# Kernel optimization log

Hardware: AMD Instinct MI355X
Metric: run time of the kernel (lower is better)

Reference implementation:

```python
import jax, jax.numpy as jnp
import numpy as np

UNITS = 2048
INPUT_DIM = 2048
BATCH = 8192


def setup_inputs() -> dict:
    key = jax.random.key(0)
    k_x, k_w = jax.random.split(key)
    inputs = jax.random.normal(k_x, (BATCH, INPUT_DIM), dtype=jnp.float32)
    # random_normal initializer in keras defaults to stddev=0.05
    w = jax.random.normal(k_w, (INPUT_DIM, UNITS), dtype=jnp.float32) * 0.05
    b = jnp.zeros((UNITS,), dtype=jnp.float32)
    return {"inputs": inputs, "w": w, "b": b}


def reference(inputs, w, b):
    # matmul + bias
    result = jnp.matmul(inputs, w) + b  # [B, units]
    # per-row: if first element > 0.5, add 1 to whole row, else subtract 1
    cond = result[:, :1] > 0.5  # [B, 1], broadcasts over row
    return jnp.where(cond, result + 1.0, result - 1.0)
```

## Files before the change

kernel.cpp:

```cpp
#include <hip/hip_runtime.h>
#include <hip/hip_bf16.h>
#include <stdint.h>

#define M_DIM 8192
#define N_DIM 2048
#define K_DIM 2048

typedef __attribute__((ext_vector_type(8))) short bf16x8;
typedef __attribute__((ext_vector_type(8))) short short8;
typedef __attribute__((ext_vector_type(4))) float f32x4;

static __device__ __forceinline__ unsigned short f2bf(float f) {
  union { float f; unsigned u; } a; a.f = f;
  unsigned u = a.u;
  u += 0x7FFFu + ((u >> 16) & 1u);
  return (unsigned short)(u >> 16);
}

static __device__ __forceinline__ void async16(void* lds, const void* g) {
  __builtin_amdgcn_global_load_lds(
      (const __attribute__((address_space(1))) unsigned int*)g,
      (__attribute__((address_space(3))) unsigned int*)lds, 16, 0, 0);
}

#define BAR()                                \
  do {                                       \
    asm volatile("" ::: "memory");           \
    __builtin_amdgcn_s_barrier();            \
    asm volatile("" ::: "memory");           \
  } while (0)
#define VMCNT(n) asm volatile("s_waitcnt vmcnt(" #n ")" ::: "memory")

__global__ __launch_bounds__(256) void k_prep(const float* __restrict__ W,
    const float* __restrict__ X, const float* __restrict__ b,
    unsigned short* __restrict__ Wt, unsigned short* __restrict__ Xb,
    float* __restrict__ adj) {
  __shared__ float smem[64 * 65];
  const int t = threadIdx.x;
  if (blockIdx.x < 1024) {
    float (*tile)[65] = (float (*)[65])smem;
    const int bx = blockIdx.x & 31;
    const int by = blockIdx.x >> 5;
    const int n0 = bx * 64, k0 = by * 64;
    #pragma unroll
    for (int i = 0; i < 16; ++i) {
      int lin = i * 256 + t;
      int rr = lin >> 6, c = lin & 63;
      tile[rr][c] = W[(size_t)(k0 + rr) * N_DIM + n0 + c];
    }
    __syncthreads();
    #pragma unroll
    for (int i = 0; i < 16; ++i) {
      int lin = i * 256 + t;
      int rr = lin >> 6, c = lin & 63;
      Wt[(size_t)(n0 + rr) * K_DIM + k0 + c] = f2bf(tile[c][rr]);
    }
  } else {
    float* wlds = smem;
    double* red2 = (double*)(smem + 2048);
    const int m0r = (blockIdx.x - 1024) * 16;
    const int w = t >> 6;
    #pragma unroll
    for (int i = 0; i < 8; ++i)
      wlds[t * 8 + i] = W[(size_t)(t * 8 + i) * N_DIM];
    __syncthreads();
    const float4 wv0 = *(const float4*)&wlds[t * 8];
    const float4 wv1 = *(const float4*)&wlds[t * 8 + 4];
    for (int rr = 0; rr < 16; ++rr) {
      const int m = m0r + rr;
      const float4* xr = (const float4*)(X + (size_t)m * K_DIM);
      float4 x0 = xr[2 * t], x1 = xr[2 * t + 1];
      short8 o;
      o[0] = (short)f2bf(x0.x); o[1] = (short)f2bf(x0.y);
      o[2] = (short)f2bf(x0.z); o[3] = (short)f2bf(x0.w);
      o[4] = (short)f2bf(x1.x); o[5] = (short)f2bf(x1.y);
      o[6] = (short)f2bf(x1.z); o[7] = (short)f2bf(x1.w);
      *(short8*)(Xb + (size_t)m * K_DIM + t * 8) = o;
      double s = (double)x0.x * wv0.x + (double)x0.y * wv0.y +
                 (double)x0.z * wv0.z + (double)x0.w * wv0.w +
                 (double)x1.x * wv1.x + (double)x1.y * wv1.y +
                 (double)x1.z * wv1.z + (double)x1.w * wv1.w;
      #pragma unroll
      for (int off = 32; off > 0; off >>= 1) s += __shfl_down(s, off, 64);
      if ((t & 63) == 0) red2[rr * 4 + w] = s;
    }
    __syncthreads();
    if (t < 16) {
      double tot = red2[t * 4] + red2[t * 4 + 1] + red2[t * 4 + 2] +
                   red2[t * 4 + 3] + (double)b[0];
      adj[m0r + t] = (tot > 0.5) ? 1.0f : -1.0f;
    }
  }
}

__device__ __forceinline__ void stage_unit(char* ldsc,
    const unsigned short* __restrict__ src, int row0, int kt,
    int isB, int sel, int wid, int l) {
  char* base = ldsc + (size_t)(kt & 1) * 65536 + (size_t)isB * 32768;
  #pragma unroll
  for (int j = 0; j < 2; ++j) {
    int s = wid * 2 + j;
    int sub_c = s & 1;
    int idx = s >> 1;
    int sub_r = isB ? ((idx & 1) + (idx >> 1) * 4 + sel * 2)
                    : ((idx & 3) + ((idx & 4) ? 8 : 0) + sel * 4);
    int grow = row0 + sub_r * 16 + (l >> 2);
    int gcol = kt * 64 + sub_c * 32 + (((l & 3) * 8) ^ ((l & 32) >> 1));
    async16(base + (size_t)(sub_r * 2 + sub_c) * 1024,
            src + (size_t)grow * K_DIM + gcol);
  }
}

__global__ __launch_bounds__(512, 1) void k_gemm8(
    const unsigned short* __restrict__ A,
    const unsigned short* __restrict__ B,
    const float* __restrict__ bias,
    const float* __restrict__ adj,
    float* __restrict__ out) {
  __shared__ unsigned short lds[2 * 2 * 256 * 64];
  char* ldsc = (char*)lds;

  const int t = threadIdx.x;
  const int wid = t >> 6, l = t & 63;
  const int wm = wid >> 2, wn = wid & 3;

  const int bid = blockIdx.x;
  const int swz = (bid & 7) * 32 + (bid >> 3);
  const int bm = swz >> 3, bn = swz & 7;
  const int m0 = bm * 256, n0 = bn * 256;

  const int r = l & 15, q = l >> 4;
  const int rdoff = (r * 64 + q * 16) ^ ((r & 8) << 2);

  const char* ab0 = ldsc;
  const char* bb0 = ldsc + 32768;
  const char* ab1 = ldsc + 65536;
  const char* bb1 = ldsc + 98304;

  f32x4 acc[8][4] = {};
  bf16x8 af0[2][4], af1[2][4], bv0[2][2], bv1[2][2];

#define STG(isB, sel, kt) \
  stage_unit(ldsc, (isB) ? B : A, (isB) ? n0 : m0, kt, isB, sel, wid, l)

#define RD_A(DST, MH, AB)                                                   \
  _Pragma("unroll") for (int mi4 = 0; mi4 < 4; ++mi4) {                     \
    const int sub_r = wm * 8 + (MH) * 4 + mi4;                              \
    _Pragma("unroll") for (int ks = 0; ks < 2; ++ks)                        \
      DST[ks][mi4] =                                                        \
          *(const bf16x8*)((AB) + (size_t)(sub_r * 2 + ks) * 1024 + rdoff); \
  }

#define RD_B(DST, NH, BB)                                                   \
  _Pragma("unroll") for (int ni2 = 0; ni2 < 2; ++ni2) {                     \
    const int sub_r = wn * 4 + (NH) * 2 + ni2;                              \
    _Pragma("unroll") for (int ks = 0; ks < 2; ++ks)                        \
      DST[ks][ni2] =                                                        \
          *(const bf16x8*)((BB) + (size_t)(sub_r * 2 + ks) * 1024 + rdoff); \
  }

#define CL(MH, NH, AF, BV)                                                  \
  __builtin_amdgcn_s_setprio(1);                                            \
  _Pragma("unroll") for (int ks = 0; ks < 2; ++ks)                          \
    _Pragma("unroll") for (int mi4 = 0; mi4 < 4; ++mi4)                     \
      _Pragma("unroll") for (int ni2 = 0; ni2 < 2; ++ni2)                   \
        acc[(MH) * 4 + mi4][(NH) * 2 + ni2] =                               \
            __builtin_amdgcn_mfma_f32_16x16x32_bf16(                        \
                AF[ks][mi4], BV[ks][ni2],                                   \
                acc[(MH) * 4 + mi4][(NH) * 2 + ni2], 0, 0, 0);              \
  __builtin_amdgcn_s_setprio(0);

#define STQ(MH, NH)                                                         \
  _Pragma("unroll") for (int mi4 = 0; mi4 < 4; ++mi4)                       \
    _Pragma("unroll") for (int ni2 = 0; ni2 < 2; ++ni2) {                   \
      const int mi = (MH) * 4 + mi4, ni = (NH) * 2 + ni2;                   \
      const int col = n0 + wn * 64 + ni * 16 + r;                           \
      const int rowb = m0 + wm * 128 + mi * 16 + q * 4;                     \
      _Pragma("unroll") for (int j = 0; j < 4; ++j)                         \
        out[(size_t)(rowb + j) * N_DIM + col] =                             \
            acc[mi][ni][j] + bias_r[ni] + adj_r[mi][j];                     \
    }

#define PH(RD_STMT, STG_STMT, CL_STMT, WAIT_STMT)                           \
  {                                                                         \
    RD_STMT;                                                                \
    STG_STMT;                                                               \
    BAR();                                                                  \
    CL_STMT;                                                                \
    WAIT_STMT;                                                              \
    BAR();                                                                  \
  }

  STG(0, 0, 0); STG(1, 0, 0); STG(1, 1, 0); STG(0, 1, 0);
  STG(0, 0, 1); STG(1, 0, 1);
  VMCNT(4);
  BAR();

  for (int i = 0; i < 15; ++i) {
    const int t1 = 2 * i + 1, t2 = 2 * i + 2, t3 = 2 * i + 3;
    PH(RD_A(af0, 0, ab0); RD_B(bv0, 0, bb0), STG(1, 1, t1),
       CL(0, 0, af0, bv0), );
    PH(RD_B(bv1, 1, bb0), STG(0, 1, t1), CL(0, 1, af0, bv1), );
    PH(RD_A(af1, 1, ab0), STG(0, 0, t2), CL(1, 0, af1, bv0), );
    PH(, STG(1, 0, t2), CL(1, 1, af1, bv1), VMCNT(4));
    PH(RD_A(af0, 0, ab1); RD_B(bv0, 0, bb1), STG(1, 1, t2),
       CL(0, 0, af0, bv0), );
    PH(RD_B(bv1, 1, bb1), STG(0, 1, t2), CL(0, 1, af0, bv1), );
    PH(RD_A(af1, 1, ab1), STG(0, 0, t3), CL(1, 0, af1, bv0), );
    PH(, STG(1, 0, t3), CL(1, 1, af1, bv1), VMCNT(4));
  }
  PH(RD_A(af0, 0, ab0); RD_B(bv0, 0, bb0), STG(1, 1, 31),
     CL(0, 0, af0, bv0), );
  PH(RD_B(bv1, 1, bb0), STG(0, 1, 31), CL(0, 1, af0, bv1), );
  PH(RD_A(af1, 1, ab0), , CL(1, 0, af1, bv0), );
  PH(, , CL(1, 1, af1, bv1), VMCNT(0));

  float4 adj_r[8];
  float bias_r[4];
  #pragma unroll
  for (int mi = 0; mi < 8; ++mi)
    adj_r[mi] = *(const float4*)&adj[m0 + wm * 128 + mi * 16 + q * 4];
  #pragma unroll
  for (int ni = 0; ni < 4; ++ni)
    bias_r[ni] = bias[n0 + wn * 64 + ni * 16 + r];

  PH(RD_A(af0, 0, ab1); RD_B(bv0, 0, bb1), , CL(0, 0, af0, bv0); STQ(0, 0), );
  PH(RD_B(bv1, 1, bb1), , CL(0, 1, af0, bv1); STQ(0, 1), );
  PH(RD_A(af1, 1, ab1), , CL(1, 0, af1, bv0); STQ(1, 0), );
  {
    CL(1, 1, af1, bv1);
    STQ(1, 1);
  }

#undef PH
#undef STQ
#undef CL
#undef RD_A
#undef RD_B
#undef STG
}

__global__ __launch_bounds__(256) void k_gemm_f32(const float* __restrict__ X,
    const float* __restrict__ W, const float* __restrict__ b,
    float* __restrict__ out) {
  __shared__ float As[16][16];
  __shared__ float Bs[16][17];
  const int bn = blockIdx.x & 127, bm = blockIdx.x >> 7;
  const int tx = threadIdx.x & 15, ty = threadIdx.x >> 4;
  const int row = bm * 16 + ty, col = bn * 16 + tx;
  float acc = 0.f;
  for (int k0 = 0; k0 < K_DIM; k0 += 16) {
    As[ty][tx] = X[(size_t)row * K_DIM + k0 + tx];
    Bs[ty][tx] = W[(size_t)(k0 + ty) * N_DIM + col];
    __syncthreads();
    #pragma unroll
    for (int kk = 0; kk < 16; ++kk) acc += As[ty][kk] * Bs[kk][tx];
    __syncthreads();
  }
  out[(size_t)row * N_DIM + col] = acc + b[col];
}

__global__ __launch_bounds__(256) void k_rowadj(float* __restrict__ out) {
  const int m = blockIdx.x;
  const float c0 = out[(size_t)m * N_DIM];
  __syncthreads();
  const float a = (c0 > 0.5f) ? 1.0f : -1.0f;
  for (int n = threadIdx.x; n < N_DIM; n += 256)
    out[(size_t)m * N_DIM + n] += a;
}

extern "C" void kernel_launch(void* const* d_in, const int* in_sizes, int n_in,
                              void* d_out, int out_size, void* d_ws, size_t ws_size,
                              hipStream_t stream) {
  const float* X = (const float*)d_in[0];
  const float* W = (const float*)d_in[1];
  const float* b = (const float*)d_in[2];
  float* out = (float*)d_out;

  const size_t XB_OFF   = 0;
  const size_t WT_OFF   = (size_t)M_DIM * K_DIM * 2;
  const size_t ADJ_OFF  = WT_OFF + (size_t)N_DIM * K_DIM * 2;
  const size_t NEED     = ADJ_OFF + (size_t)M_DIM * 4;

  if (ws_size >= NEED) {
    unsigned short* Xb  = (unsigned short*)((char*)d_ws + XB_OFF);
    unsigned short* Wt  = (unsigned short*)((char*)d_ws + WT_OFF);
    float* adj  = (float*)((char*)d_ws + ADJ_OFF);
    k_prep<<<dim3(1536), dim3(256), 0, stream>>>(W, X, b, Wt, Xb, adj);
    k_gemm8<<<dim3((M_DIM / 256) * (N_DIM / 256)), dim3(512), 0, stream>>>(
        Xb, Wt, b, adj, out);
  } else {
    k_gemm_f32<<<dim3((M_DIM / 16) * (N_DIM / 16)), dim3(256), 0, stream>>>(
        X, W, b, out);
    k_rowadj<<<dim3(M_DIM), dim3(256), 0, stream>>>(out);
  }
}
```

Before: 88.54 us.

## Replace 256x256 eight-phase GEMM with 256x128 tile, K=32 steps, higher occupancy

Swaps the 256x256-tile GEMM, which used a deep 8-phase software pipeline and 128KB of LDS at one block per CU, for a 256x128 tile. The new kernel uses 32-wide K steps with a simple double buffer in 48KB of LDS and launch bounds that allow several blocks per CU. The aim is to hide latency through occupancy rather than hand scheduling and to give the grid more blocks. In exchange, each output needs more global and LDS traffic, and there are twice as many barriers per unit of K work.

```diff
diff --git a/kernel.cpp b/kernel.cpp
--- a/kernel.cpp
+++ b/kernel.cpp
@@ -93,151 +93,119 @@
   }
 }
 
-__device__ __forceinline__ void stage_unit(char* ldsc,
-    const unsigned short* __restrict__ src, int row0, int kt,
-    int isB, int sel, int wid, int l) {
-  char* base = ldsc + (size_t)(kt & 1) * 65536 + (size_t)isB * 32768;
-  #pragma unroll
-  for (int j = 0; j < 2; ++j) {
-    int s = wid * 2 + j;
-    int sub_c = s & 1;
-    int idx = s >> 1;
-    int sub_r = isB ? ((idx & 1) + (idx >> 1) * 4 + sel * 2)
-                    : ((idx & 3) + ((idx & 4) ? 8 : 0) + sel * 4);
-    int grow = row0 + sub_r * 16 + (l >> 2);
-    int gcol = kt * 64 + sub_c * 32 + (((l & 3) * 8) ^ ((l & 32) >> 1));
-    async16(base + (size_t)(sub_r * 2 + sub_c) * 1024,
-            src + (size_t)grow * K_DIM + gcol);
-  }
-}
-
-__global__ __launch_bounds__(512, 1) void k_gemm8(
+__global__ __launch_bounds__(512, 4) void k_gemm2(
     const unsigned short* __restrict__ A,
     const unsigned short* __restrict__ B,
     const float* __restrict__ bias,
     const float* __restrict__ adj,
     float* __restrict__ out) {
-  __shared__ unsigned short lds[2 * 2 * 256 * 64];
+  __shared__ unsigned short lds[2 * 12288];
   char* ldsc = (char*)lds;
 
   const int t = threadIdx.x;
   const int wid = t >> 6, l = t & 63;
-  const int wm = wid >> 2, wn = wid & 3;
+  const int wm = wid >> 1, wn = wid & 1;
 
   const int bid = blockIdx.x;
-  const int swz = (bid & 7) * 32 + (bid >> 3);
-  const int bm = swz >> 3, bn = swz & 7;
-  const int m0 = bm * 256, n0 = bn * 256;
+  const int swz = (bid & 7) * 64 + (bid >> 3);
+  const int bm = swz >> 4, bn = swz & 15;
+  const int m0 = bm * 256, n0 = bn * 128;
 
   const int r = l & 15, q = l >> 4;
   const int rdoff = (r * 64 + q * 16) ^ ((r & 8) << 2);
-
-  const char* ab0 = ldsc;
-  const char* bb0 = ldsc + 32768;
-  const char* ab1 = ldsc + 65536;
-  const char* bb1 = ldsc + 98304;
-
-  f32x4 acc[8][4] = {};
-  bf16x8 af0[2][4], af1[2][4], bv0[2][2], bv1[2][2];
-
-#define STG(isB, sel, kt) \
-  stage_unit(ldsc, (isB) ? B : A, (isB) ? n0 : m0, kt, isB, sel, wid, l)
-
-#define RD_A(DST, MH, AB)                                                   \
-  _Pragma("unroll") for (int mi4 = 0; mi4 < 4; ++mi4) {                     \
-    const int sub_r = wm * 8 + (MH) * 4 + mi4;                              \
-    _Pragma("unroll") for (int ks = 0; ks < 2; ++ks)                        \
-      DST[ks][mi4] =                                                        \
-          *(const bf16x8*)((AB) + (size_t)(sub_r * 2 + ks) * 1024 + rdoff); \
-  }
-
-#define RD_B(DST, NH, BB)                                                   \
-  _Pragma("unroll") for (int ni2 = 0; ni2 < 2; ++ni2) {                     \
-    const int sub_r = wn * 4 + (NH) * 2 + ni2;                              \
-    _Pragma("unroll") for (int ks = 0; ks < 2; ++ks)                        \
-      DST[ks][ni2] =                                                        \
-          *(const bf16x8*)((BB) + (size_t)(sub_r * 2 + ks) * 1024 + rdoff); \
-  }
-
-#define CL(MH, NH, AF, BV)                                                  \
-  __builtin_amdgcn_s_setprio(1);                                            \
-  _Pragma("unroll") for (int ks = 0; ks < 2; ++ks)                          \
-    _Pragma("unroll") for (int mi4 = 0; mi4 < 4; ++mi4)                     \
-      _Pragma("unroll") for (int ni2 = 0; ni2 < 2; ++ni2)                   \
-        acc[(MH) * 4 + mi4][(NH) * 2 + ni2] =                               \
-            __builtin_amdgcn_mfma_f32_16x16x32_bf16(                        \
-                AF[ks][mi4], BV[ks][ni2],                                   \
-                acc[(MH) * 4 + mi4][(NH) * 2 + ni2], 0, 0, 0);              \
-  __builtin_amdgcn_s_setprio(0);
-
-#define STQ(MH, NH)                                                         \
-  _Pragma("unroll") for (int mi4 = 0; mi4 < 4; ++mi4)                       \
-    _Pragma("unroll") for (int ni2 = 0; ni2 < 2; ++ni2) {                   \
-      const int mi = (MH) * 4 + mi4, ni = (NH) * 2 + ni2;                   \
-      const int col = n0 + wn * 64 + ni * 16 + r;                           \
-      const int rowb = m0 + wm * 128 + mi * 16 + q * 4;                     \
-      _Pragma("unroll") for (int j = 0; j < 4; ++j)                         \
-        out[(size_t)(rowb + j) * N_DIM + col] =                             \
-            acc[mi][ni][j] + bias_r[ni] + adj_r[mi][j];                     \
-    }
-
-#define PH(RD_STMT, STG_STMT, CL_STMT, WAIT_STMT)                           \
-  {                                                                         \
-    RD_STMT;                                                                \
-    STG_STMT;                                                               \
-    BAR();                                                                  \
-    CL_STMT;                                                                \
-    WAIT_STMT;                                                              \
-    BAR();                                                                  \
-  }
-
-  STG(0, 0, 0); STG(1, 0, 0); STG(1, 1, 0); STG(0, 1, 0);
-  STG(0, 0, 1); STG(1, 0, 1);
-  VMCNT(4);
+  const int grow_l = l >> 2;
+  const int gcol_l = ((l & 3) * 8) ^ ((l & 32) >> 1);
+
+  f32x4 acc[4][4] = {};
+  bf16x8 af[4], bv[4];
+
+#define STAGE_STEP(kt)                                                      \
+  do {                                                                      \
+    char* base = ldsc + (size_t)((kt) & 1) * 24576;                         \
+    const int gc = (kt) * 32 + gcol_l;                                      \
+    async16(base + (size_t)wid * 1024,                                      \
+            A + (size_t)(m0 + wid * 16 + grow_l) * K_DIM + gc);             \
+    async16(base + (size_t)(wid + 8) * 1024,                                \
+            A + (size_t)(m0 + 128 + wid * 16 + grow_l) * K_DIM + gc);       \
+    async16(base + 16384 + (size_t)wid * 1024,                              \
+            B + (size_t)(n0 + wid * 16 + grow_l) * K_DIM + gc);             \
+  } while (0)
+
+#define RD_FRAGS(BUF)                                                       \
+  do {                                                                      \
+    _Pragma("unroll") for (int mi = 0; mi < 4; ++mi)                        \
+      af[mi] = *(const bf16x8*)((BUF) + (size_t)(wm * 4 + mi) * 1024 +      \
+                                rdoff);                                     \
+    _Pragma("unroll") for (int ni = 0; ni < 4; ++ni)                        \
+      bv[ni] = *(const bf16x8*)((BUF) + 16384 +                             \
+                                (size_t)(wn * 4 + ni) * 1024 + rdoff);      \
+  } while (0)
+
+#define MF(NLO)                                                             \
+  do {                                                                      \
+    __builtin_amdgcn_s_setprio(1);                                          \
+    _Pragma("unroll") for (int mi = 0; mi < 4; ++mi)                        \
+      _Pragma("unroll") for (int nn = 0; nn < 2; ++nn)                      \
+        acc[mi][(NLO) + nn] = __builtin_amdgcn_mfma_f32_16x16x32_bf16(      \
+            af[mi], bv[(NLO) + nn], acc[mi][(NLO) + nn], 0, 0, 0);          \
+    __builtin_amdgcn_s_setprio(0);                                          \
+  } while (0)
+
+  STAGE_STEP(0);
+  STAGE_STEP(1);
+  VMCNT(3);
   BAR();
 
-  for (int i = 0; i < 15; ++i) {
-    const int t1 = 2 * i + 1, t2 = 2 * i + 2, t3 = 2 * i + 3;
-    PH(RD_A(af0, 0, ab0); RD_B(bv0, 0, bb0), STG(1, 1, t1),
-       CL(0, 0, af0, bv0), );
-    PH(RD_B(bv1, 1, bb0), STG(0, 1, t1), CL(0, 1, af0, bv1), );
-    PH(RD_A(af1, 1, ab0), STG(0, 0, t2), CL(1, 0, af1, bv0), );
-    PH(, STG(1, 0, t2), CL(1, 1, af1, bv1), VMCNT(4));
-    PH(RD_A(af0, 0, ab1); RD_B(bv0, 0, bb1), STG(1, 1, t2),
-       CL(0, 0, af0, bv0), );
-    PH(RD_B(bv1, 1, bb1), STG(0, 1, t2), CL(0, 1, af0, bv1), );
-    PH(RD_A(af1, 1, ab1), STG(0, 0, t3), CL(1, 0, af1, bv0), );
-    PH(, STG(1, 0, t3), CL(1, 1, af1, bv1), VMCNT(4));
-  }
-  PH(RD_A(af0, 0, ab0); RD_B(bv0, 0, bb0), STG(1, 1, 31),
-     CL(0, 0, af0, bv0), );
-  PH(RD_B(bv1, 1, bb0), STG(0, 1, 31), CL(0, 1, af0, bv1), );
-  PH(RD_A(af1, 1, ab0), , CL(1, 0, af1, bv0), );
-  PH(, , CL(1, 1, af1, bv1), VMCNT(0));
-
-  float4 adj_r[8];
+  for (int j = 0; j < 62; ++j) {
+    const char* buf = ldsc + (size_t)(j & 1) * 24576;
+    RD_FRAGS(buf);
+    MF(0);
+    BAR();
+    STAGE_STEP(j + 2);
+    MF(2);
+    VMCNT(3);
+    BAR();
+  }
+  {
+    const char* buf = ldsc;
+    RD_FRAGS(buf);
+    MF(0);
+    BAR();
+    MF(2);
+    VMCNT(0);
+    BAR();
+  }
+  {
+    const char* buf = ldsc + 24576;
+    RD_FRAGS(buf);
+    MF(0);
+    MF(2);
+  }
+
+#undef MF
+#undef RD_FRAGS
+#undef STAGE_STEP
+
+  float4 adj_r[4];
   float bias_r[4];
   #pragma unroll
-  for (int mi = 0; mi < 8; ++mi)
-    adj_r[mi] = *(const float4*)&adj[m0 + wm * 128 + mi * 16 + q * 4];
+  for (int mi = 0; mi < 4; ++mi)
+    adj_r[mi] = *(const float4*)&adj[m0 + wm * 64 + mi * 16 + q * 4];
   #pragma unroll
   for (int ni = 0; ni < 4; ++ni)
     bias_r[ni] = bias[n0 + wn * 64 + ni * 16 + r];
-
-  PH(RD_A(af0, 0, ab1); RD_B(bv0, 0, bb1), , CL(0, 0, af0, bv0); STQ(0, 0), );
-  PH(RD_B(bv1, 1, bb1), , CL(0, 1, af0, bv1); STQ(0, 1), );
-  PH(RD_A(af1, 1, ab1), , CL(1, 0, af1, bv0); STQ(1, 0), );
-  {
-    CL(1, 1, af1, bv1);
-    STQ(1, 1);
-  }
-
-#undef PH
-#undef STQ
-#undef CL
-#undef RD_A
-#undef RD_B
-#undef STG
+  #pragma unroll
+  for (int mi = 0; mi < 4; ++mi) {
+    const int rowb = m0 + wm * 64 + mi * 16 + q * 4;
+    #pragma unroll
+    for (int ni = 0; ni < 4; ++ni) {
+      const int col = n0 + wn * 64 + ni * 16 + r;
+      #pragma unroll
+      for (int j = 0; j < 4; ++j)
+        out[(size_t)(rowb + j) * N_DIM + col] =
+            acc[mi][ni][j] + bias_r[ni] + adj_r[mi][j];
+    }
+  }
 }
 
 __global__ __launch_bounds__(256) void k_gemm_f32(const float* __restrict__ X,
@@ -287,7 +255,7 @@
     unsigned short* Wt  = (unsigned short*)((char*)d_ws + WT_OFF);
     float* adj  = (float*)((char*)d_ws + ADJ_OFF);
     k_prep<<<dim3(1536), dim3(256), 0, stream>>>(W, X, b, Wt, Xb, adj);
-    k_gemm8<<<dim3((M_DIM / 256) * (N_DIM / 256)), dim3(512), 0, stream>>>(
+    k_gemm2<<<dim3((M_DIM / 256) * (N_DIM / 128)), dim3(512), 0, stream>>>(
         Xb, Wt, b, adj, out);
   } else {
     k_gemm_f32<<<dim3((M_DIM / 16) * (N_DIM / 16)), dim3(256), 0, stream>>>(
```

Result: slower. 99.41 us (+12.3%).

## Load B fragments directly from global into registers, bypassing LDS

Applied to the files above, without the earlier changes.

Each warp now loads its B (weight) fragments straight from global memory into registers, double-buffered across k-tiles. Only A is staged through LDS, so shared memory per block is halved and the LDS reads for B go away. In exchange, B is fetched redundantly by the two warp rows (wm) with uncoalesced 16-byte strided loads, it uses more registers, and the vmcnt wait accounting gets more complicated.

```diff
diff --git a/kernel.cpp b/kernel.cpp
--- a/kernel.cpp
+++ b/kernel.cpp
@@ -93,17 +93,16 @@
   }
 }
 
-__device__ __forceinline__ void stage_unit(char* ldsc,
+__device__ __forceinline__ void stage_unitA(char* ldsc,
     const unsigned short* __restrict__ src, int row0, int kt,
-    int isB, int sel, int wid, int l) {
-  char* base = ldsc + (size_t)(kt & 1) * 65536 + (size_t)isB * 32768;
+    int sel, int wid, int l) {
+  char* base = ldsc + (size_t)(kt & 1) * 32768;
   #pragma unroll
   for (int j = 0; j < 2; ++j) {
     int s = wid * 2 + j;
     int sub_c = s & 1;
     int idx = s >> 1;
-    int sub_r = isB ? ((idx & 1) + (idx >> 1) * 4 + sel * 2)
-                    : ((idx & 3) + ((idx & 4) ? 8 : 0) + sel * 4);
+    int sub_r = (idx & 3) + ((idx & 4) ? 8 : 0) + sel * 4;
     int grow = row0 + sub_r * 16 + (l >> 2);
     int gcol = kt * 64 + sub_c * 32 + (((l & 3) * 8) ^ ((l & 32) >> 1));
     async16(base + (size_t)(sub_r * 2 + sub_c) * 1024,
@@ -111,13 +110,13 @@
   }
 }
 
-__global__ __launch_bounds__(512, 1) void k_gemm8(
+__global__ __launch_bounds__(512, 1) void k_gemm8b(
     const unsigned short* __restrict__ A,
     const unsigned short* __restrict__ B,
     const float* __restrict__ bias,
     const float* __restrict__ adj,
     float* __restrict__ out) {
-  __shared__ unsigned short lds[2 * 2 * 256 * 64];
+  __shared__ unsigned short lds[2 * 256 * 64];
   char* ldsc = (char*)lds;
 
   const int t = threadIdx.x;
@@ -133,15 +132,21 @@
   const int rdoff = (r * 64 + q * 16) ^ ((r & 8) << 2);
 
   const char* ab0 = ldsc;
-  const char* bb0 = ldsc + 32768;
-  const char* ab1 = ldsc + 65536;
-  const char* bb1 = ldsc + 98304;
+  const char* ab1 = ldsc + 32768;
+
+  const unsigned short* Bln = B + (size_t)(n0 + wn * 64 + r) * K_DIM + q * 8;
 
   f32x4 acc[8][4] = {};
-  bf16x8 af0[2][4], af1[2][4], bv0[2][2], bv1[2][2];
-
-#define STG(isB, sel, kt) \
-  stage_unit(ldsc, (isB) ? B : A, (isB) ? n0 : m0, kt, isB, sel, wid, l)
+  bf16x8 af0[2][4], af1[2][4];
+  bf16x8 bvE[2][4], bvO[2][4];
+
+#define STG_A(sel, kt) stage_unitA(ldsc, A, m0, kt, sel, wid, l)
+
+#define GB(DST, kt)                                                         \
+  _Pragma("unroll") for (int nj = 0; nj < 4; ++nj)                          \
+    _Pragma("unroll") for (int ks = 0; ks < 2; ++ks)                        \
+      DST[ks][nj] = *(const bf16x8*)(Bln + (size_t)(nj * 16) * K_DIM +      \
+                                     (kt) * 64 + ks * 32);
 
 #define RD_A(DST, MH, AB)                                                   \
   _Pragma("unroll") for (int mi4 = 0; mi4 < 4; ++mi4) {                     \
@@ -149,14 +154,6 @@
     _Pragma("unroll") for (int ks = 0; ks < 2; ++ks)                        \
       DST[ks][mi4] =                                                        \
           *(const bf16x8*)((AB) + (size_t)(sub_r * 2 + ks) * 1024 + rdoff); \
-  }
-
-#define RD_B(DST, NH, BB)                                                   \
-  _Pragma("unroll") for (int ni2 = 0; ni2 < 2; ++ni2) {                     \
-    const int sub_r = wn * 4 + (NH) * 2 + ni2;                              \
-    _Pragma("unroll") for (int ks = 0; ks < 2; ++ks)                        \
-      DST[ks][ni2] =                                                        \
-          *(const bf16x8*)((BB) + (size_t)(sub_r * 2 + ks) * 1024 + rdoff); \
   }
 
 #define CL(MH, NH, AF, BV)                                                  \
@@ -166,7 +163,7 @@
       _Pragma("unroll") for (int ni2 = 0; ni2 < 2; ++ni2)                   \
         acc[(MH) * 4 + mi4][(NH) * 2 + ni2] =                               \
             __builtin_amdgcn_mfma_f32_16x16x32_bf16(                        \
-                AF[ks][mi4], BV[ks][ni2],                                   \
+                AF[ks][mi4], BV[ks][(NH) * 2 + ni2],                        \
                 acc[(MH) * 4 + mi4][(NH) * 2 + ni2], 0, 0, 0);              \
   __builtin_amdgcn_s_setprio(0);
 
@@ -191,29 +188,26 @@
     BAR();                                                                  \
   }
 
-  STG(0, 0, 0); STG(1, 0, 0); STG(1, 1, 0); STG(0, 1, 0);
-  STG(0, 0, 1); STG(1, 0, 1);
-  VMCNT(4);
+  GB(bvE, 0);
+  STG_A(0, 0); STG_A(1, 0); STG_A(0, 1);
+  VMCNT(0);
   BAR();
 
   for (int i = 0; i < 15; ++i) {
     const int t1 = 2 * i + 1, t2 = 2 * i + 2, t3 = 2 * i + 3;
-    PH(RD_A(af0, 0, ab0); RD_B(bv0, 0, bb0), STG(1, 1, t1),
-       CL(0, 0, af0, bv0), );
-    PH(RD_B(bv1, 1, bb0), STG(0, 1, t1), CL(0, 1, af0, bv1), );
-    PH(RD_A(af1, 1, ab0), STG(0, 0, t2), CL(1, 0, af1, bv0), );
-    PH(, STG(1, 0, t2), CL(1, 1, af1, bv1), VMCNT(4));
-    PH(RD_A(af0, 0, ab1); RD_B(bv0, 0, bb1), STG(1, 1, t2),
-       CL(0, 0, af0, bv0), );
-    PH(RD_B(bv1, 1, bb1), STG(0, 1, t2), CL(0, 1, af0, bv1), );
-    PH(RD_A(af1, 1, ab1), STG(0, 0, t3), CL(1, 0, af1, bv0), );
-    PH(, STG(1, 0, t3), CL(1, 1, af1, bv1), VMCNT(4));
-  }
-  PH(RD_A(af0, 0, ab0); RD_B(bv0, 0, bb0), STG(1, 1, 31),
-     CL(0, 0, af0, bv0), );
-  PH(RD_B(bv1, 1, bb0), STG(0, 1, 31), CL(0, 1, af0, bv1), );
-  PH(RD_A(af1, 1, ab0), , CL(1, 0, af1, bv0), );
-  PH(, , CL(1, 1, af1, bv1), VMCNT(0));
+    PH(RD_A(af0, 0, ab0), GB(bvO, t1), CL(0, 0, af0, bvE), );
+    PH(, STG_A(1, t1), CL(0, 1, af0, bvE), VMCNT(10));
+    PH(RD_A(af1, 1, ab0), STG_A(0, t2), CL(1, 0, af1, bvE), );
+    PH(, , CL(1, 1, af1, bvE), );
+    PH(RD_A(af0, 0, ab1), GB(bvE, t2), CL(0, 0, af0, bvO), );
+    PH(, STG_A(1, t2), CL(0, 1, af0, bvO), VMCNT(12));
+    PH(RD_A(af1, 1, ab1), STG_A(0, t3), CL(1, 0, af1, bvO), );
+    PH(, , CL(1, 1, af1, bvO), VMCNT(12));
+  }
+  PH(RD_A(af0, 0, ab0), GB(bvO, 31), CL(0, 0, af0, bvE), );
+  PH(, STG_A(1, 31), CL(0, 1, af0, bvE), );
+  PH(RD_A(af1, 1, ab0), , CL(1, 0, af1, bvE), );
+  PH(, , CL(1, 1, af1, bvE), VMCNT(0));
 
   float4 adj_r[8];
   float bias_r[4];
@@ -224,11 +218,11 @@
   for (int ni = 0; ni < 4; ++ni)
     bias_r[ni] = bias[n0 + wn * 64 + ni * 16 + r];
 
-  PH(RD_A(af0, 0, ab1); RD_B(bv0, 0, bb1), , CL(0, 0, af0, bv0); STQ(0, 0), );
-  PH(RD_B(bv1, 1, bb1), , CL(0, 1, af0, bv1); STQ(0, 1), );
-  PH(RD_A(af1, 1, ab1), , CL(1, 0, af1, bv0); STQ(1, 0), );
+  PH(RD_A(af0, 0, ab1), , CL(0, 0, af0, bvO); STQ(0, 0), );
+  PH(, , CL(0, 1, af0, bvO); STQ(0, 1), );
+  PH(RD_A(af1, 1, ab1), , CL(1, 0, af1, bvO); STQ(1, 0), );
   {
-    CL(1, 1, af1, bv1);
+    CL(1, 1, af1, bvO);
     STQ(1, 1);
   }
 
@@ -236,8 +230,8 @@
 #undef STQ
 #undef CL
 #undef RD_A
-#undef RD_B
-#undef STG
+#undef GB
+#undef STG_A
 }
 
 __global__ __launch_bounds__(256) void k_gemm_f32(const float* __restrict__ X,
@@ -287,7 +281,7 @@
     unsigned short* Wt  = (unsigned short*)((char*)d_ws + WT_OFF);
     float* adj  = (float*)((char*)d_ws + ADJ_OFF);
     k_prep<<<dim3(1536), dim3(256), 0, stream>>>(W, X, b, Wt, Xb, adj);
-    k_gemm8<<<dim3((M_DIM / 256) * (N_DIM / 256)), dim3(512), 0, stream>>>(
+    k_gemm8b<<<dim3((M_DIM / 256) * (N_DIM / 256)), dim3(512), 0, stream>>>(
         Xb, Wt, b, adj, out);
   } else {
     k_gemm_f32<<<dim3((M_DIM / 16) * (N_DIM / 16)), dim3(256), 0, stream>>>(
```

New measurement: 123.1 us. +39.0%, slower.
